# Performance work log

Hardware: AMD Instinct MI355X
Metric: run time of the kernel (lower is better)

Reference implementation:

```python
import jax, jax.numpy as jnp
import numpy as np

POOL = (7, 7)


def crop_and_resize(image, boxes, box_idx, crop_size):
    """Faithful jnp port of tf.image.crop_and_resize (bilinear, extrapolation_value=0).

    image: [B, H, W, C]; boxes: [N, 4] normalized (y1, x1, y2, x2); box_idx: [N] int.
    Returns [N, ph, pw, C].
    """
    H, W = image.shape[1], image.shape[2]
    ph, pw = crop_size
    y1, x1, y2, x2 = boxes[:, 0], boxes[:, 1], boxes[:, 2], boxes[:, 3]
    iy = jnp.arange(ph, dtype=image.dtype)
    ix = jnp.arange(pw, dtype=image.dtype)
    # sample coords in source-pixel space, TF convention for crop_size > 1
    ys = y1[:, None] * (H - 1) + iy[None, :] * ((y2 - y1)[:, None] * (H - 1) / (ph - 1))  # [N, ph]
    xs = x1[:, None] * (W - 1) + ix[None, :] * ((x2 - x1)[:, None] * (W - 1) / (pw - 1))  # [N, pw]
    vy = (ys >= 0) & (ys <= H - 1)
    vx = (xs >= 0) & (xs <= W - 1)
    y0 = jnp.floor(ys)
    x0 = jnp.floor(xs)
    wy = (ys - y0)[:, :, None, None]   # [N, ph, 1, 1]
    wx = (xs - x0)[:, None, :, None]   # [N, 1, pw, 1]
    y0i = jnp.clip(y0, 0, H - 1).astype(jnp.int32)
    y1i = jnp.clip(y0 + 1, 0, H - 1).astype(jnp.int32)  # when ys is integral, wy==0 so clamp is harmless
    x0i = jnp.clip(x0, 0, W - 1).astype(jnp.int32)
    x1i = jnp.clip(x0 + 1, 0, W - 1).astype(jnp.int32)
    b = box_idx[:, None, None]

    def g(yi, xi):
        return image[b, yi[:, :, None], xi[:, None, :], :]  # [N, ph, pw, C]

    top = g(y0i, x0i) * (1 - wx) + g(y0i, x1i) * wx
    bot = g(y1i, x0i) * (1 - wx) + g(y1i, x1i) * wx
    out = top * (1 - wy) + bot * wy
    valid = (vy[:, :, None] & vx[:, None, :])[..., None]
    return jnp.where(valid, out, jnp.zeros((), image.dtype))


def setup_inputs() -> dict:
    key = jax.random.key(0)
    kb, kp, k3, k4, k5 = jax.random.split(key, 5)
    B, N, C = 2, 1000, 256
    # valid normalized boxes: per-axis sorted uniforms -> y1 <= y2, x1 <= x2
    raw = jax.random.uniform(kb, (B, N, 2, 2), dtype=jnp.float32)  # [..., (y|x), (lo,hi)]
    raw = jnp.sort(raw, axis=-1)
    boxes = jnp.stack([raw[..., 0, 0], raw[..., 1, 0], raw[..., 0, 1], raw[..., 1, 1]], axis=-1)
    return {
        "boxes": boxes,
        "positive_indices": jax.random.randint(kp, (B, N), 0, 2, dtype=jnp.int32),
        "p3": jax.random.normal(k3, (B, 128, 128, C), dtype=jnp.float32),
        "p4": jax.random.normal(k4, (B, 64, 64, C), dtype=jnp.float32),
        "p5": jax.random.normal(k5, (B, 32, 32, C), dtype=jnp.float32),
        "config": 0,
    }


def reference(boxes, positive_indices, p3, p4, p5, config):
    B, N = boxes.shape[0], boxes.shape[1]
    ph, pw = POOL
    h = boxes[..., 2] - boxes[..., 0]
    w = boxes[..., 3] - boxes[..., 1]
    # roi_level = clip(ceil(5 + log2(h*w)), 3, 5); clip in float first (log2(0) -> -inf)
    lvl = jnp.ceil(5.0 + jnp.log(h * w) / jnp.log(2.0))
    roi_level = jnp.clip(lvl, 3.0, 5.0).astype(jnp.int32)  # [B, N]
    boxes_flat = jax.lax.stop_gradient(boxes.reshape(B * N, 4))  # boxes get no grad in original
    lvl_flat = roi_level.reshape(B * N)
    box_idx = jnp.repeat(jnp.arange(B, dtype=jnp.int32), N)
    C = p3.shape[-1]
    pooled = jnp.zeros((B * N, ph, pw, C), dtype=p3.dtype)
    for level, feat in zip((3, 4, 5), (p3, p4, p5)):
        crop = crop_and_resize(feat, boxes_flat, box_idx, POOL)
        mask = (lvl_flat == level)[:, None, None, None]
        pooled = jnp.where(mask, crop, pooled)
    return pooled.reshape(B, N, ph, pw, C)
```

## Files before the change

### kernel.cpp

```cpp
#include <hip/hip_runtime.h>
#include <math.h>


#define N_PER_B 1000
#define NBOX    2000
#define CCH     256
#define PH      7
#define PW      7
#define WAVES_PER_BLOCK 4
#define TOTAL_WAVES (NBOX * PH)

typedef float nfloat4 __attribute__((ext_vector_type(4)));

__global__ __launch_bounds__(256, 3) void pyramid_roi_align_kernel(
    const float* __restrict__ boxes,
    const float* __restrict__ p3,
    const float* __restrict__ p4,
    const float* __restrict__ p5,
    float* __restrict__ out)
{
    const int wave = blockIdx.x * WAVES_PER_BLOCK + (threadIdx.x >> 6);
    const int lane = threadIdx.x & 63;
    const int c    = lane * 4;

    const int box = wave / PH;
    const int iy  = wave - box * PH;

    const float y1 = boxes[box * 4 + 0];
    const float x1 = boxes[box * 4 + 1];
    const float y2 = boxes[box * 4 + 2];
    const float x2 = boxes[box * 4 + 3];
    const float h  = y2 - y1;
    const float w  = x2 - x1;

    const float lvl  = ceilf(5.0f + logf(h * w) / 0.69314718055994530942f);
    const float lvlc = fminf(fmaxf(lvl, 3.0f), 5.0f);
    const int level  = (int)lvlc;

    const float* feat;
    int H;
    if (level <= 3)      { feat = p3; H = 128; }
    else if (level == 4) { feat = p4; H = 64;  }
    else                 { feat = p5; H = 32;  }
    const int W = H;

    const int b = (box >= N_PER_B) ? 1 : 0;
    feat += (size_t)b * H * W * CCH;

    const float Hm1 = (float)(H - 1);
    const float Wm1 = (float)(W - 1);

    const float ys = y1 * Hm1 + (float)iy * (h * Hm1 / 6.0f);
    const bool  vy = (ys >= 0.0f) && (ys <= Hm1);

    const float y0f  = floorf(ys);
    const float wy   = ys - y0f;
    const float omwy = 1.0f - wy;

    const int y0i = (int)fminf(fmaxf(y0f,        0.0f), Hm1);
    const int y1i = (int)fminf(fmaxf(y0f + 1.0f, 0.0f), Hm1);

    const float* row0 = feat + (size_t)y0i * W * CCH + c;
    const float* row1 = feat + (size_t)y1i * W * CCH + c;

    const float xstep = w * Wm1 / 6.0f;

    nfloat4 v00[PW], v01[PW], v10[PW], v11[PW];
    float   wxv[PW];
    bool    vxv[PW];

#pragma unroll
    for (int ix = 0; ix < PW; ++ix) {
        const float xs = x1 * Wm1 + (float)ix * xstep;
        vxv[ix] = (xs >= 0.0f) && (xs <= Wm1);
        const float x0f = floorf(xs);
        wxv[ix] = xs - x0f;
        const int x0i = (int)fminf(fmaxf(x0f,        0.0f), Wm1);
        const int x1i = (int)fminf(fmaxf(x0f + 1.0f, 0.0f), Wm1);
        v00[ix] = *(const nfloat4*)(row0 + (size_t)x0i * CCH);
        v01[ix] = *(const nfloat4*)(row0 + (size_t)x1i * CCH);
        v10[ix] = *(const nfloat4*)(row1 + (size_t)x0i * CCH);
        v11[ix] = *(const nfloat4*)(row1 + (size_t)x1i * CCH);
    }

    float* dst_base = out + ((size_t)box * (PH * PW) + (size_t)iy * PW) * CCH + c;

#pragma unroll
    for (int ix = 0; ix < PW; ++ix) {
        const float wx   = wxv[ix];
        const float omwx = 1.0f - wx;

        nfloat4 res = (v00[ix] * omwx + v01[ix] * wx) * omwy
                    + (v10[ix] * omwx + v11[ix] * wx) * wy;

        if (!(vy && vxv[ix])) res = (nfloat4)0.0f;

        __builtin_nontemporal_store(res, (nfloat4*)(dst_base + (size_t)ix * CCH));
    }
}

extern "C" void kernel_launch(void* const* d_in, const int* in_sizes, int n_in,
                              void* d_out, int out_size, void* d_ws, size_t ws_size,
                              hipStream_t stream) {
    const float* boxes = (const float*)d_in[0];
    const float* p3 = (const float*)d_in[2];
    const float* p4 = (const float*)d_in[3];
    const float* p5 = (const float*)d_in[4];
    float* out = (float*)d_out;

    const int grid = TOTAL_WAVES / WAVES_PER_BLOCK;
    hipLaunchKernelGGL(pyramid_roi_align_kernel, dim3(grid), dim3(256), 0, stream,
                       boxes, p3, p4, p5, out);
}
```

Before: 169.6 us.

## Sort boxes by batch, level and spatial bucket; remap blocks across XCDs for L2 locality

Adds a single-block pre-pass kernel that buckets the 2000 boxes by batch, pyramid level and a coarse 8x8 center grid, then writes a permutation to workspace. The main kernel reads boxes in that order and swizzles block indices so consecutive logical blocks land on the same XCD. Spatially nearby boxes then share feature rows in that XCD's L2, which should cut HBM reads. The cost is an extra serial single-block launch and an indirect box lookup, and the gain depends on the workspace being large enough for the sort to run.

```diff
diff --git a/kernel.cpp b/kernel.cpp
--- a/kernel.cpp
+++ b/kernel.cpp
@@ -9,22 +9,75 @@
 #define PW      7
 #define WAVES_PER_BLOCK 4
 #define TOTAL_WAVES (NBOX * PH)
+#define GRID_MAIN   ((TOTAL_WAVES + WAVES_PER_BLOCK - 1) / WAVES_PER_BLOCK + 7) / 8 * 8
+#define NBUCKET 512
 
 typedef float nfloat4 __attribute__((ext_vector_type(4)));
+
+__global__ __launch_bounds__(1024) void sort_boxes_kernel(
+    const float* __restrict__ boxes, int* __restrict__ order)
+{
+    __shared__ int hist[NBUCKET];
+    __shared__ int offs[NBUCKET];
+    __shared__ int keys[NBOX];
+
+    const int t = threadIdx.x;
+    if (t < NBUCKET) hist[t] = 0;
+    __syncthreads();
+
+    for (int i = t; i < NBOX; i += 1024) {
+        const float y1 = boxes[4 * i + 0];
+        const float x1 = boxes[4 * i + 1];
+        const float y2 = boxes[4 * i + 2];
+        const float x2 = boxes[4 * i + 3];
+        const float h = y2 - y1, w = x2 - x1;
+        const float lvl = ceilf(5.0f + logf(h * w) / 0.69314718055994530942f);
+        const int level = (int)fminf(fmaxf(lvl, 3.0f), 5.0f);
+        const int b  = (i >= N_PER_B) ? 1 : 0;
+        int cy = (int)((y1 + y2) * 4.0f); cy = cy < 0 ? 0 : (cy > 7 ? 7 : cy);
+        int cx = (int)((x1 + x2) * 4.0f); cx = cx < 0 ? 0 : (cx > 7 ? 7 : cx);
+        const int key = (((b * 3 + (level - 3)) * 8 + cy) * 8 + cx);
+        keys[i] = key;
+        atomicAdd(&hist[key], 1);
+    }
+    __syncthreads();
+
+    if (t < NBUCKET) offs[t] = hist[t];
+    __syncthreads();
+    for (int d = 1; d < NBUCKET; d <<= 1) {
+        int v = 0;
+        if (t < NBUCKET && t >= d) v = offs[t - d];
+        __syncthreads();
+        if (t < NBUCKET) offs[t] += v;
+        __syncthreads();
+    }
+    if (t < NBUCKET) hist[t] = offs[t] - hist[t];
+    __syncthreads();
+
+    for (int i = t; i < NBOX; i += 1024) {
+        const int pos = atomicAdd(&hist[keys[i]], 1);
+        order[pos] = i;
+    }
+}
 
 __global__ __launch_bounds__(256, 3) void pyramid_roi_align_kernel(
     const float* __restrict__ boxes,
     const float* __restrict__ p3,
     const float* __restrict__ p4,
     const float* __restrict__ p5,
+    const int*   __restrict__ order,
     float* __restrict__ out)
 {
-    const int wave = blockIdx.x * WAVES_PER_BLOCK + (threadIdx.x >> 6);
+    const int nb_per_xcd = GRID_MAIN / 8;
+    const int vb   = (blockIdx.x & 7) * nb_per_xcd + (blockIdx.x >> 3);
+    const int wave = vb * WAVES_PER_BLOCK + (threadIdx.x >> 6);
+    if (wave >= TOTAL_WAVES) return;
     const int lane = threadIdx.x & 63;
     const int c    = lane * 4;
 
-    const int box = wave / PH;
-    const int iy  = wave - box * PH;
+    const int sidx = wave / PH;
+    const int iy   = wave - sidx * PH;
+    const int box  = order ? order[sidx] : sidx;
 
     const float y1 = boxes[box * 4 + 0];
     const float x1 = boxes[box * 4 + 1];
@@ -108,7 +161,13 @@
     const float* p5 = (const float*)d_in[4];
     float* out = (float*)d_out;
 
-    const int grid = TOTAL_WAVES / WAVES_PER_BLOCK;
-    hipLaunchKernelGGL(pyramid_roi_align_kernel, dim3(grid), dim3(256), 0, stream,
-                       boxes, p3, p4, p5, out);
+    int* order = nullptr;
+    if (ws_size >= NBOX * sizeof(int)) {
+        order = (int*)d_ws;
+        hipLaunchKernelGGL(sort_boxes_kernel, dim3(1), dim3(1024), 0, stream,
+                           boxes, order);
+    }
+
+    hipLaunchKernelGGL(pyramid_roi_align_kernel, dim3(GRID_MAIN), dim3(256), 0, stream,
+                       boxes, p3, p4, p5, order, out);
 }
```

After: 175.9 us. +3.7%, slower.
